# Kernel tuning notes

Hardware: AMD Instinct MI355X
Metric: run time of the kernel (lower is better)

The kernel has to match this reference:

```python
import jax, jax.numpy as jnp
import numpy as np

B, N, FIN = 32, 1024, 6
KCHEB = 3
CLASS_NUM = 40


def _pairwise_adj(x):
    # x: [B, N, D] -> exp(-squared_euclidean_dist) adjacency [B, N, N]
    inner = jnp.einsum('bnd,bmd->bnm', x, x)
    sq = jnp.sum(x * x, axis=-1)
    d2 = sq[:, :, None] - 2.0 * inner + sq[:, None, :]
    return jnp.exp(-d2)


def _get_laplacian(adj):
    # normalized Laplacian: I - D^{-1/2} A D^{-1/2}
    deg = jnp.sum(adj, axis=-1)                       # [B, N]
    d_is = 1.0 / jnp.sqrt(deg)                        # [B, N]
    eye = jnp.eye(adj.shape[-1], dtype=adj.dtype)
    return eye - d_is[:, :, None] * adj * d_is[:, None, :]


def _cheb_conv(x, L, W, b):
    # Chebyshev graph conv: sum_k T_k(L) x W_k + b;  W: [K, Fin, Fout]
    x0 = x
    x1 = jnp.einsum('bnm,bmf->bnf', L, x0)
    out = jnp.einsum('bnf,fg->bng', x0, W[0]) + jnp.einsum('bnf,fg->bng', x1, W[1])
    xk_2, xk_1 = x0, x1
    for k in range(2, W.shape[0]):
        xk = 2.0 * jnp.einsum('bnm,bmf->bnf', L, xk_1) - xk_2
        out = out + jnp.einsum('bnf,fg->bng', xk, W[k])
        xk_2, xk_1 = xk_1, xk
    return out + b


def setup_inputs() -> dict:
    key = jax.random.key(0)
    ks = jax.random.split(key, 16)

    def w(k, shape, fan_in):
        return jax.random.normal(k, shape, dtype=jnp.float32) / np.sqrt(fan_in)

    return {
        'x': jax.random.normal(ks[0], (B, N, FIN), dtype=jnp.float32),
        'W1': w(ks[1], (KCHEB, 6, 128), 6 * KCHEB),
        'b1': jnp.zeros((128,), jnp.float32),
        'W2': w(ks[2], (KCHEB, 128, 512), 128 * KCHEB),
        'b2': jnp.zeros((512,), jnp.float32),
        'W3': w(ks[3], (KCHEB, 512, 1024), 512 * KCHEB),
        'b3': jnp.zeros((1024,), jnp.float32),
        'fc1_w': w(ks[4], (1024, 512), 1024),
        'fc1_b': jnp.zeros((512,), jnp.float32),
        'fc2_w': w(ks[5], (512, 128), 512),
        'fc2_b': jnp.zeros((128,), jnp.float32),
        'fc3_w': w(ks[6], (128, CLASS_NUM), 128),
        'fc3_b': jnp.zeros((CLASS_NUM,), jnp.float32),
    }


def reference(x, W1, b1, W2, b2, W3, b3, fc1_w, fc1_b, fc2_w, fc2_b, fc3_w, fc3_b):
    # Laplacians are computed under torch.no_grad in the original
    L = _get_laplacian(_pairwise_adj(x))
    out = jax.nn.relu(_cheb_conv(x, L, W1, b1))        # [B, N, 128]

    L = _get_laplacian(_pairwise_adj(out))
    out = jax.nn.relu(_cheb_conv(out, L, W2, b2))      # [B, N, 512]

    L = _get_laplacian(_pairwise_adj(out))
    out = jax.nn.relu(_cheb_conv(out, L, W3, b3))      # [B, N, 1024]

    out = jnp.max(out, axis=1)                          # global max pool -> [B, 1024]
    out = jax.nn.relu(out @ fc1_w + fc1_b)              # dropout is identity at eval
    out = jax.nn.relu(out @ fc2_w + fc2_b)
    out = out @ fc3_w + fc3_b                           # [B, CLASS_NUM]
    return out
```

## Files before the change

### kernel.cpp

```cpp
#include <hip/hip_runtime.h>
#include <cstddef>


#define NN 1024

typedef unsigned short ushort_t;
typedef __bf16 bf16x8 __attribute__((ext_vector_type(8)));
typedef float f32x4 __attribute__((ext_vector_type(4)));

__device__ inline ushort_t f2bf(float f) {
    unsigned int u = __float_as_uint(f);
    u = (u + 0x7fffu + ((u >> 16) & 1u)) >> 16;
    return (ushort_t)u;
}
__device__ inline float bf2f(ushort_t s) {
    return __uint_as_float(((unsigned int)s) << 16);
}

__device__ __attribute__((always_inline)) inline void gld16(
    const ushort_t* g, ushort_t* l) {
    __builtin_amdgcn_global_load_lds(
        (__attribute__((address_space(1))) void*)(ushort_t*)g,
        (__attribute__((address_space(3))) void*)l, 16, 0, 0);
}

__global__ void zero_kernel(float* __restrict__ p, int n) {
    int i = blockIdx.x * blockDim.x + threadIdx.x;
    if (i < n) p[i] = 0.f;
}

__global__ __launch_bounds__(256) void wconvT_kernel(
    const float* __restrict__ W, ushort_t* __restrict__ Wt, int Fi, int Fo, int Ks) {
    int p = blockIdx.z;
    int k0 = blockIdx.y * 64, g0 = blockIdx.x * 64;
    __shared__ float T[64][65];
    int t = threadIdx.x;
#pragma unroll
    for (int q = 0; q < 16; ++q) {
        int kr = (t >> 6) + 4 * q, gc = t & 63;
        int k = k0 + kr, g = g0 + gc;
        T[kr][gc] = (k < Fi && g < Fo) ? W[((size_t)p * Fi + k) * Fo + g] : 0.f;
    }
    __syncthreads();
#pragma unroll
    for (int q = 0; q < 16; ++q) {
        int gr = (t >> 6) + 4 * q, kc = t & 63;
        int g = g0 + gr, k = k0 + kc;
        if (g < Fo && k < Ks)
            Wt[((size_t)p * Fo + g) * Ks + k] = f2bf(T[kc][gr]);
    }
}

__global__ __launch_bounds__(256) void prep2_kernel(
    const float* __restrict__ X, ushort_t* __restrict__ hi, ushort_t* __restrict__ lo,
    ushort_t* __restrict__ Xt, float* __restrict__ sq, int F, int Fp, int bsh) {
    int L = blockIdx.x;
    int b = L & ((1 << bsh) - 1), n0 = (L >> bsh) * 64;
    int t = threadIdx.x;
    __shared__ float T[64][65];
    __shared__ float red[4][64];
    const float* Xb = X + ((size_t)b * NN + n0) * F;
    float sacc = 0.f;

    for (int f0 = 0; f0 < Fp; f0 += 64) {
        __syncthreads();
#pragma unroll
        for (int p = 0; p < 16; ++p) {
            int nr = (t >> 6) + 4 * p, fc = t & 63;
            int f = f0 + fc;
            T[nr][fc] = (f < F) ? Xb[(size_t)nr * F + f] : 0.f;
        }
        __syncthreads();
#pragma unroll
        for (int p = 0; p < 16; ++p) {
            int nr = (t >> 6) + 4 * p, fc = t & 63;
            int f = f0 + fc;
            if (f < Fp) {
                float x = T[nr][fc];
                ushort_t h = f2bf(x);
                size_t off = ((size_t)b * NN + n0 + nr) * Fp + f;
                hi[off] = h;
                lo[off] = f2bf(x - bf2f(h));
            }
        }
#pragma unroll
        for (int p = 0; p < 16; ++p) {
            int fr = (t >> 6) + 4 * p;
            int f = f0 + fr;
            if (f < F)
                Xt[((size_t)b * Fp + f) * NN + n0 + (t & 63)] = f2bf(T[t & 63][fr]);
        }
        {
            int nl = t & 63, fq = t >> 6;
#pragma unroll
            for (int fc = 0; fc < 16; ++fc) {
                float v = T[nl][fq * 16 + fc];
                sacc += v * v;
            }
        }
    }
    red[t >> 6][t & 63] = sacc;
    __syncthreads();
    if (t < 64)
        sq[(size_t)b * NN + n0 + t] = red[0][t] + red[1][t] + red[2][t] + red[3][t];
}

__global__ __launch_bounds__(256) void adj_kernel(
    const ushort_t* __restrict__ hi, const ushort_t* __restrict__ lo,
    const float* __restrict__ sq, ushort_t* __restrict__ Abf,
    float* __restrict__ deg_part, int Fp, int bsh, int BCv) {
    int t = threadIdx.x;
    int L = blockIdx.x;
    int b = L & ((1 << bsh) - 1);
    int rest = L >> bsh;
    int ti = 0;
    while (rest >= 8 - ti) { rest -= 8 - ti; ++ti; }
    int tj = ti + rest;
    int n0 = ti * 128, m0 = tj * 128;
    const ushort_t* Hb = hi + (size_t)b * NN * Fp;
    const ushort_t* Lb = lo + (size_t)b * NN * Fp;
    ushort_t* Ab = Abf + (size_t)b * NN * NN;
    const float* sqb = sq + (size_t)b * NN;

    int lane = t & 63, quad = lane >> 4, l16 = lane & 15, wave = t >> 6;
    int rowoff = (wave >> 1) * 64, coloff = (wave & 1) * 64;

    __shared__ __align__(16) ushort_t smem[40960];

    f32x4 acc[4][4];
#pragma unroll
    for (int i = 0; i < 4; ++i)
#pragma unroll
        for (int j = 0; j < 4; ++j) acc[i][j] = (f32x4){0.f, 0.f, 0.f, 0.f};

    int rr0 = t >> 2, kq = (t & 3) * 8;
    int rr1 = rr0 + 64;
    const ushort_t* pAh0 = Hb + (size_t)(n0 + rr0) * Fp + kq;
    const ushort_t* pAh1 = Hb + (size_t)(n0 + rr1) * Fp + kq;
    const ushort_t* pAl0 = Lb + (size_t)(n0 + rr0) * Fp + kq;
    const ushort_t* pAl1 = Lb + (size_t)(n0 + rr1) * Fp + kq;
    const ushort_t* pBh0 = Hb + (size_t)(m0 + rr0) * Fp + kq;
    const ushort_t* pBh1 = Hb + (size_t)(m0 + rr1) * Fp + kq;
    const ushort_t* pBl0 = Lb + (size_t)(m0 + rr0) * Fp + kq;
    const ushort_t* pBl1 = Lb + (size_t)(m0 + rr1) * Fp + kq;
    int o0 = rr0 * 40 + kq, o1 = rr1 * 40 + kq;

    {
        *(uint4*)&smem[o0]         = *(const uint4*)pAh0;
        *(uint4*)&smem[o1]         = *(const uint4*)pAh1;
        *(uint4*)&smem[5120 + o0]  = *(const uint4*)pAl0;
        *(uint4*)&smem[5120 + o1]  = *(const uint4*)pAl1;
        *(uint4*)&smem[10240 + o0] = *(const uint4*)pBh0;
        *(uint4*)&smem[10240 + o1] = *(const uint4*)pBh1;
        *(uint4*)&smem[15360 + o0] = *(const uint4*)pBl0;
        *(uint4*)&smem[15360 + o1] = *(const uint4*)pBl1;
    }
    __syncthreads();

    int NIT = Fp >> 5;
    for (int it = 0; it < NIT; ++it) {
        int cur = (it & 1) * 20480;
        int nxt = 20480 - cur;
        uint4 rh0, rh1, rl0, rl1, sh0, sh1, sl0, sl1;
        if (it + 1 < NIT) {
            int k = (it + 1) * 32;
            rh0 = *(const uint4*)(pAh0 + k); rh1 = *(const uint4*)(pAh1 + k);
            rl0 = *(const uint4*)(pAl0 + k); rl1 = *(const uint4*)(pAl1 + k);
            sh0 = *(const uint4*)(pBh0 + k); sh1 = *(const uint4*)(pBh1 + k);
            sl0 = *(const uint4*)(pBl0 + k); sl1 = *(const uint4*)(pBl1 + k);
        }
        ushort_t* Ah = smem + cur;
        ushort_t* Al = smem + cur + 5120;
        ushort_t* Bh = smem + cur + 10240;
        ushort_t* Bl = smem + cur + 15360;
        bf16x8 ah[4], al[4], bh[4], bl[4];
#pragma unroll
        for (int i = 0; i < 4; ++i) {
            ah[i] = *(const bf16x8*)&Ah[(rowoff + i * 16 + l16) * 40 + quad * 8];
            al[i] = *(const bf16x8*)&Al[(rowoff + i * 16 + l16) * 40 + quad * 8];
        }
#pragma unroll
        for (int j = 0; j < 4; ++j) {
            bh[j] = *(const bf16x8*)&Bh[(coloff + j * 16 + l16) * 40 + quad * 8];
            bl[j] = *(const bf16x8*)&Bl[(coloff + j * 16 + l16) * 40 + quad * 8];
        }
#pragma unroll
        for (int i = 0; i < 4; ++i)
#pragma unroll
            for (int j = 0; j < 4; ++j) {
                acc[i][j] = __builtin_amdgcn_mfma_f32_16x16x32_bf16(al[i], bh[j], acc[i][j], 0, 0, 0);
                acc[i][j] = __builtin_amdgcn_mfma_f32_16x16x32_bf16(ah[i], bl[j], acc[i][j], 0, 0, 0);
                acc[i][j] = __builtin_amdgcn_mfma_f32_16x16x32_bf16(ah[i], bh[j], acc[i][j], 0, 0, 0);
            }
        if (it + 1 < NIT) {
            *(uint4*)&smem[nxt + o0]         = rh0;
            *(uint4*)&smem[nxt + o1]         = rh1;
            *(uint4*)&smem[nxt + 5120 + o0]  = rl0;
            *(uint4*)&smem[nxt + 5120 + o1]  = rl1;
            *(uint4*)&smem[nxt + 10240 + o0] = sh0;
            *(uint4*)&smem[nxt + 10240 + o1] = sh1;
            *(uint4*)&smem[nxt + 15360 + o0] = sl0;
            *(uint4*)&smem[nxt + 15360 + o1] = sl1;
        }
        __syncthreads();
    }

    bool offdiag = (ti != tj);
    float rs[4][4];
    float cs[4] = {0.f, 0.f, 0.f, 0.f};
#pragma unroll
    for (int i = 0; i < 4; ++i)
#pragma unroll
        for (int r = 0; r < 4; ++r) rs[i][r] = 0.f;

#pragma unroll
    for (int j = 0; j < 4; ++j) {
        int ml = coloff + j * 16 + l16;
        int m = m0 + ml;
        float sm = sqb[m];
#pragma unroll
        for (int i = 0; i < 4; ++i) {
#pragma unroll
            for (int r = 0; r < 4; ++r) {
                int nl = rowoff + i * 16 + quad * 4 + r;
                int n = n0 + nl;
                float v = __expf(2.f * acc[i][j][r] - sqb[n] - sm);
                Ab[(size_t)n * NN + m] = f2bf(v);
                rs[i][r] += v;
                if (offdiag) {
                    cs[j] += v;
                    smem[ml * 128 + (((nl >> 3) ^ (ml & 7)) << 3) + (nl & 7)] = f2bf(v);
                }
            }
        }
    }
    int slot = tj * 2 + (wave & 1);
#pragma unroll
    for (int i = 0; i < 4; ++i)
#pragma unroll
        for (int r = 0; r < 4; ++r) {
            float s = rs[i][r];
            s += __shfl_xor(s, 1);
            s += __shfl_xor(s, 2);
            s += __shfl_xor(s, 4);
            s += __shfl_xor(s, 8);
            if (l16 == 0)
                deg_part[((size_t)slot * BCv + b) * NN + n0 + rowoff + i * 16 + quad * 4 + r] = s;
        }

    if (offdiag) {
#pragma unroll
        for (int j = 0; j < 4; ++j) {
            float s = cs[j];
            s += __shfl_xor(s, 16);
            s += __shfl_xor(s, 32);
            cs[j] = s;
        }
        if (quad == 0) {
#pragma unroll
            for (int j = 0; j < 4; ++j)
                deg_part[((size_t)(ti * 2 + (wave >> 1)) * BCv + b) * NN +
                         m0 + coloff + j * 16 + l16] = cs[j];
        }
        __syncthreads();
        for (int s2 = t; s2 < 2048; s2 += 256) {
            int ml = s2 >> 4, oct = s2 & 15;
            uint4 v4 = *(const uint4*)&smem[ml * 128 + ((oct ^ (ml & 7)) << 3)];
            *(uint4*)(Ab + (size_t)(m0 + ml) * NN + n0 + oct * 8) = v4;
        }
    }
}

__global__ __launch_bounds__(256) void disscale_kernel(
    ushort_t* __restrict__ Xt, const float* __restrict__ deg_part,
    float* __restrict__ dis, int Fp, int bsh, int BCv) {
    int L = blockIdx.x;
    int b = L & ((1 << bsh) - 1), n0 = (L >> bsh) * 64;
    int t = threadIdx.x;
    __shared__ float dloc[64];
    if (t < 64) {
        float s = 0.f;
#pragma unroll
        for (int k = 0; k < 16; ++k) s += deg_part[((size_t)k * BCv + b) * NN + n0 + t];
        float d = rsqrtf(s);
        dloc[t] = d;
        dis[(size_t)b * NN + n0 + t] = d;
    }
    __syncthreads();
    int lane = t & 63, fq = t >> 6;
    float d = dloc[lane];
    ushort_t* Xb = Xt + (size_t)b * Fp * NN + n0 + lane;
    for (int f = fq; f < Fp; f += 4) {
        size_t off = (size_t)f * NN;
        Xb[off] = f2bf(bf2f(Xb[off]) * d);
    }
}

__global__ __launch_bounds__(256) void lx_kernel(
    const ushort_t* __restrict__ Abf, const float* __restrict__ dis,
    const ushort_t* __restrict__ in_t, const ushort_t* __restrict__ x0t,
    ushort_t* __restrict__ out_t, ushort_t* __restrict__ out_b,
    int F, int Fp, int mode, int ft, int bsh) {
    int t = threadIdx.x;
    int L = blockIdx.x;
    int b = L & ((1 << bsh) - 1);
    int rest = L >> bsh;
    int m0 = (rest % ft) * 128;
    int n0 = (rest / ft) * 64;
    const ushort_t* Ain = in_t + (size_t)b * Fp * NN;
    const ushort_t* Ab = Abf + (size_t)b * NN * NN;

    int lane = t & 63, quad = lane >> 4, l16 = lane & 15, wave = t >> 6;
    int rowoff = wave * 32;

    __shared__ __align__(16) ushort_t smem[18432];

    f32x4 acc[2][4];
#pragma unroll
    for (int i = 0; i < 2; ++i)
#pragma unroll
        for (int j = 0; j < 4; ++j) acc[i][j] = (f32x4){0.f, 0.f, 0.f, 0.f};

    int lr = lane >> 2, lk = (lane & 3) * 8;
    int rbase = wave * 32;
    const ushort_t* gA = Ain + (size_t)(m0 + rbase + lr) * NN + lk;
    const ushort_t* gB = Ab + (size_t)(n0 + wave * 16 + lr) * NN + lk;

#define LX_STAGE(BOFF, CI)                                            \
    {                                                                 \
        int k_ = (CI) * 32;                                           \
        ushort_t* As_ = smem + (BOFF);                                \
        gld16(gA + k_, As_ + rbase * 32);                             \
        gld16(gA + (size_t)16 * NN + k_, As_ + rbase * 32 + 512);     \
        gld16(gB + k_, As_ + 4096 + wave * 16 * 32);                  \
    }
#define LX_COMP(BOFF)                                                            \
    {                                                                            \
        ushort_t* As_ = smem + (BOFF);                                           \
        ushort_t* Bs_ = As_ + 4096;                                              \
        bf16x8 af[2], bfv[4];                                                    \
        _Pragma("unroll")                                                        \
        for (int i = 0; i < 2; ++i)                                              \
            af[i] = *(const bf16x8*)&As_[(rowoff + i * 16 + l16) * 32 + quad * 8]; \
        _Pragma("unroll")                                                        \
        for (int j = 0; j < 4; ++j)                                              \
            bfv[j] = *(const bf16x8*)&Bs_[(j * 16 + l16) * 32 + quad * 8];       \
        _Pragma("unroll")                                                        \
        for (int i = 0; i < 2; ++i)                                              \
            _Pragma("unroll")                                                    \
            for (int j = 0; j < 4; ++j)                                          \
                acc[i][j] = __builtin_amdgcn_mfma_f32_16x16x32_bf16(af[i], bfv[j], acc[i][j], 0, 0, 0); \
    }

    LX_STAGE(0, 0);
    LX_STAGE(6144, 1);
    int cur = 0;
    for (int ci = 0; ci < 32; ++ci) {
        if (ci < 31) { asm volatile("s_waitcnt vmcnt(3)" ::: "memory"); }
        else         { asm volatile("s_waitcnt vmcnt(0)" ::: "memory"); }
        __builtin_amdgcn_s_barrier();
        asm volatile("" ::: "memory");
        if (ci + 2 < 32) {
            int noff = cur + 12288; if (noff >= 18432) noff -= 18432;
            LX_STAGE(noff, ci + 2);
        }
        LX_COMP(cur);
        cur += 6144; if (cur >= 18432) cur = 0;
    }
#undef LX_STAGE
#undef LX_COMP
    __syncthreads();

#pragma unroll
    for (int j = 0; j < 4; ++j) {
        int nl = j * 16 + l16;
        int n = n0 + nl;
        float dn = dis[(size_t)b * NN + n];
        float inv = 1.f / dn;
        float dn2 = dn * dn;
#pragma unroll
        for (int i = 0; i < 2; ++i) {
#pragma unroll
            for (int r = 0; r < 4; ++r) {
                int fl = rowoff + i * 16 + quad * 4 + r;
                int f = m0 + fl;
                float o = 0.f;
                if (f < F) {
                    float a = acc[i][j][r];
                    size_t off = (size_t)f * NN + n;
                    float xin = bf2f(Ain[off]);
                    if (mode == 0) {
                        out_t[(size_t)b * Fp * NN + off] = f2bf(xin - dn2 * a);
                        o = inv * xin - dn * a;
                    } else {
                        float x0 = bf2f(x0t[(size_t)b * Fp * NN + off]);
                        o = inv * (2.f * xin - x0) - 2.f * dn * a;
                    }
                }
                smem[nl * 128 + (((fl >> 3) ^ (nl & 7)) << 3) + (fl & 7)] = f2bf(o);
            }
        }
    }
    __syncthreads();
    for (int s2 = t; s2 < 1024; s2 += 256) {
        int nl = s2 >> 4, oct = s2 & 15;
        int fg = m0 + oct * 8;
        if (fg < Fp) {
            uint4 v = *(const uint4*)&smem[nl * 128 + ((oct ^ (nl & 7)) << 3)];
            *(uint4*)(out_b + ((size_t)b * NN + n0 + nl) * Fp + fg) = v;
        }
    }
}

__global__ __launch_bounds__(512) void proj_kernel(
    const ushort_t* __restrict__ X0, const ushort_t* __restrict__ X1,
    const ushort_t* __restrict__ X2, const ushort_t* __restrict__ Wt,
    const float* __restrict__ bias, float* __restrict__ O, float* __restrict__ pool,
    int Fp, int Fo, int b0, int n_g, int bsh) {
    int t = threadIdx.x;
    int L = blockIdx.x;
    int c = L & ((1 << bsh) - 1);
    int rest = L >> bsh;
    int g0 = (rest % n_g) * 128;
    int r0 = (c * 4 + rest / n_g) * 256;
    int lane = t & 63, quad = lane >> 4, l16 = lane & 15, wave = t >> 6;
    int rowoff = (wave >> 1) * 64, coloff = (wave & 1) * 64;

    __shared__ __align__(16) ushort_t smem[36864];

    f32x4 acc[4][4];
#pragma unroll
    for (int i = 0; i < 4; ++i)
#pragma unroll
        for (int j = 0; j < 4; ++j) acc[i][j] = (f32x4){0.f, 0.f, 0.f, 0.f};

    int lr = lane >> 2, lk = (lane & 3) * 8;
    int nk = Fp >> 5;
    int NIT = 3 * nk;
    size_t FoFp = (size_t)Fo * Fp;
    size_t r16 = (size_t)16 * Fp;

#define PJ_STAGE(BOFF, CI)                                                    \
    {                                                                         \
        int p_ = (CI) / nk;                                                   \
        int k_ = ((CI) - p_ * nk) * 32 + lk;                                  \
        const ushort_t* Xp_ = (p_ == 0) ? X0 : ((p_ == 1) ? X1 : X2);         \
        const ushort_t* ga_ = Xp_ + (size_t)(r0 + wave * 32 + lr) * Fp + k_;  \
        const ushort_t* gb_ = Wt + (size_t)p_ * FoFp +                        \
                              (size_t)(g0 + wave * 16 + lr) * Fp + k_;        \
        ushort_t* As_ = smem + (BOFF) + wave * 1024;                          \
        ushort_t* Bs_ = smem + (BOFF) + 8192 + wave * 512;                    \
        gld16(ga_, As_);                                                      \
        gld16(ga_ + r16, As_ + 512);                                          \
        gld16(gb_, Bs_);                                                      \
    }
#define PJ_COMP(BOFF)                                                           \
    {                                                                           \
        ushort_t* As_ = smem + (BOFF);                                          \
        ushort_t* Bs_ = As_ + 8192;                                             \
        bf16x8 af[4], bfv[4];                                                   \
        _Pragma("unroll")                                                       \
        for (int i = 0; i < 4; ++i)                                             \
            af[i] = *(const bf16x8*)&As_[(rowoff + i * 16 + l16) * 32 + quad * 8];  \
        _Pragma("unroll")                                                       \
        for (int j = 0; j < 4; ++j)                                             \
            bfv[j] = *(const bf16x8*)&Bs_[(coloff + j * 16 + l16) * 32 + quad * 8]; \
        _Pragma("unroll")                                                       \
        for (int i = 0; i < 4; ++i)                                             \
            _Pragma("unroll")                                                   \
            for (int j = 0; j < 4; ++j)                                         \
                acc[i][j] = __builtin_amdgcn_mfma_f32_16x16x32_bf16(af[i], bfv[j], acc[i][j], 0, 0, 0); \
    }

    PJ_STAGE(0, 0);
    PJ_STAGE(12288, 1);
    int cur = 0;
    for (int ci = 0; ci < NIT; ++ci) {
        if (ci < NIT - 1) { asm volatile("s_waitcnt vmcnt(3)" ::: "memory"); }
        else              { asm volatile("s_waitcnt vmcnt(0)" ::: "memory"); }
        __builtin_amdgcn_s_barrier();
        asm volatile("" ::: "memory");
        if (ci + 2 < NIT) {
            int noff = cur + 24576; if (noff >= 36864) noff -= 36864;
            PJ_STAGE(noff, ci + 2);
        }
        PJ_COMP(cur);
        cur += 12288; if (cur >= 36864) cur = 0;
    }
#undef PJ_STAGE
#undef PJ_COMP

    float bias_l[4];
#pragma unroll
    for (int j = 0; j < 4; ++j) bias_l[j] = bias[g0 + coloff + j * 16 + l16];

    if (O) {
#pragma unroll
        for (int i = 0; i < 4; ++i) {
#pragma unroll
            for (int r = 0; r < 4; ++r) {
                int row = r0 + rowoff + i * 16 + quad * 4 + r;
#pragma unroll
                for (int j = 0; j < 4; ++j) {
                    int g = g0 + coloff + j * 16 + l16;
                    O[(size_t)row * Fo + g] = fmaxf(acc[i][j][r] + bias_l[j], 0.f);
                }
            }
        }
    } else {
        float mj[4];
#pragma unroll
        for (int j = 0; j < 4; ++j) {
            float m = 0.f;
#pragma unroll
            for (int i = 0; i < 4; ++i)
#pragma unroll
                for (int r = 0; r < 4; ++r)
                    m = fmaxf(m, acc[i][j][r] + bias_l[j]);
            m = fmaxf(m, 0.f);
            m = fmaxf(m, __shfl_xor(m, 16));
            m = fmaxf(m, __shfl_xor(m, 32));
            mj[j] = m;
        }
        if (quad == 0) {
            int smp = b0 + (r0 >> 10);
#pragma unroll
            for (int j = 0; j < 4; ++j)
                atomicMax((int*)&pool[(size_t)smp * 1024 + g0 + coloff + j * 16 + l16],
                          __float_as_int(mj[j]));
        }
    }
}

__global__ __launch_bounds__(256) void fc_kernel(
    const float* __restrict__ In, const float* __restrict__ W,
    const float* __restrict__ bias, float* __restrict__ out,
    int K, int Nout, int relu) {
    int r = blockIdx.y;
    int c0 = blockIdx.x * 64;
    int t = threadIdx.x;
    int cl = t & 63, ks = t >> 6;
    int c = c0 + cl;
    int kchunk = K >> 2;
    int k0 = ks * kchunk, k1 = k0 + kchunk;
    float s = 0.f;
    if (c < Nout) {
        const float* ip = In + (size_t)r * K;
        const float* wp = W + c;
#pragma unroll 4
        for (int k = k0; k < k1; ++k) s += ip[k] * wp[(size_t)k * Nout];
    }
    __shared__ float red[4][64];
    red[ks][cl] = s;
    __syncthreads();
    if (t < 64 && c0 + t < Nout) {
        float v = red[0][t] + red[1][t] + red[2][t] + red[3][t] + bias[c0 + t];
        if (relu) v = fmaxf(v, 0.f);
        out[(size_t)r * Nout + c0 + t] = v;
    }
}

extern "C" void kernel_launch(void* const* d_in, const int* in_sizes, int n_in,
                              void* d_out, int out_size, void* d_ws, size_t ws_size,
                              hipStream_t stream) {
    const float* x    = (const float*)d_in[0];
    const float* W1   = (const float*)d_in[1];
    const float* b1   = (const float*)d_in[2];
    const float* W2   = (const float*)d_in[3];
    const float* b2   = (const float*)d_in[4];
    const float* W3   = (const float*)d_in[5];
    const float* b3   = (const float*)d_in[6];
    const float* fc1w = (const float*)d_in[7];
    const float* fc1b = (const float*)d_in[8];
    const float* fc2w = (const float*)d_in[9];
    const float* fc2b = (const float*)d_in[10];
    const float* fc3w = (const float*)d_in[11];
    const float* fc3b = (const float*)d_in[12];
    float* out = (float*)d_out;

    auto need = [](size_t BCv) -> size_t {
        size_t us = (size_t)BCv * 1024;
        return 2 * (us * 1024) + 10 * (us * 512) + 2 * 1781760ull +
               4 * (us * 128) + 4 * (us * 512) + 4 * us + 64 * us + 4 * us +
               4 * (32768ull + 16384 + 4096) + 256;
    };
    int BCv = (ws_size >= need(32)) ? 32 : (ws_size >= need(16)) ? 16 : 8;
    int NCH = 32 / BCv;
    int bsh = (BCv == 32) ? 5 : (BCv == 16) ? 4 : 3;

    size_t usc = (size_t)BCv * 1024;
    size_t Asz = usc * 1024;
    size_t SLv = usc * 512;
    ushort_t* Abf  = (ushort_t*)d_ws;
    ushort_t* X0hi = Abf + Asz;
    ushort_t* X0lo = X0hi + SLv;
    ushort_t* X0t  = X0lo + SLv;
    ushort_t* X1t  = X0t + SLv;
    ushort_t* X1b  = X1t + SLv;
    ushort_t* Wt   = X1b + SLv;
    float* O1   = (float*)(Wt + 1781760);
    float* O2   = O1 + usc * 128;
    float* sq   = O2 + usc * 512;
    float* degp = sq + usc;
    float* dis  = degp + 16 * usc;
    float* pool = dis + usc;
    float* f1   = pool + 32768;
    float* f2   = f1 + 16384;
    ushort_t* X2b = X0lo;

    wconvT_kernel<<<dim3(2, 1, 3), 256, 0, stream>>>(W1, Wt, 6, 128, 32);
    wconvT_kernel<<<dim3(8, 2, 3), 256, 0, stream>>>(W2, Wt + 12288, 128, 512, 128);
    wconvT_kernel<<<dim3(16, 8, 3), 256, 0, stream>>>(W3, Wt + 208896, 512, 1024, 512);
    zero_kernel<<<128, 256, 0, stream>>>(pool, 32768);

    for (int c = 0; c < NCH; ++c) {
        int b0 = c * BCv;
        struct LayerDef {
            const float* X; int F, Fp, Fo;
            const ushort_t* Wtl; const float* bias; float* O;
        };
        LayerDef L[3] = {
            { x + (size_t)b0 * NN * 6, 6,   32,  128,  Wt,          b1, O1 },
            { O1,                      128, 128, 512,  Wt + 12288,  b2, O2 },
            { O2,                      512, 512, 1024, Wt + 208896, b3, nullptr },
        };
        for (int li = 0; li < 3; ++li) {
            LayerDef& Ld = L[li];
            int F = Ld.F, Fp = Ld.Fp;
            int ft = (F + 127) / 128;
            int n_g = Ld.Fo / 128;
            prep2_kernel<<<16 * BCv, 256, 0, stream>>>(Ld.X, X0hi, X0lo, X0t, sq, F, Fp, bsh);
            adj_kernel<<<36 * BCv, 256, 0, stream>>>(X0hi, X0lo, sq, Abf, degp, Fp, bsh, BCv);
            disscale_kernel<<<16 * BCv, 256, 0, stream>>>(X0t, degp, dis, Fp, bsh, BCv);
            lx_kernel<<<ft * 16 * BCv, 256, 0, stream>>>(
                Abf, dis, X0t, nullptr, X1t, X1b, F, Fp, 0, ft, bsh);
            lx_kernel<<<ft * 16 * BCv, 256, 0, stream>>>(
                Abf, dis, X1t, X0t, nullptr, X2b, F, Fp, 1, ft, bsh);
            proj_kernel<<<n_g * 4 * BCv, 512, 0, stream>>>(
                X0hi, X1b, X2b, Ld.Wtl, Ld.bias, Ld.O, pool, Fp, Ld.Fo, b0, n_g, bsh);
        }
    }

    fc_kernel<<<dim3(8, 32), 256, 0, stream>>>(pool, fc1w, fc1b, f1, 1024, 512, 1);
    fc_kernel<<<dim3(2, 32), 256, 0, stream>>>(f1, fc2w, fc2b, f2, 512, 128, 1);
    fc_kernel<<<dim3(1, 32), 256, 0, stream>>>(f2, fc3w, fc3b, out, 128, 40, 0);
}
```

Measured before the change: 959.1 us.

## Emit next-layer bf16 hi/lo split directly from projection epilogue

The projection kernel now writes its ReLU output as bf16 hi/lo pairs instead of fp32, straight into rotating workspace slots. The next layer's prep kernel reads those pairs back and rebuilds the values rather than re-splitting fp32 and rewriting hi/lo. This removes the fp32 intermediate buffers, cuts some memory traffic and shrinks the workspace requirement, which may allow a larger batch chunk. The cost is a buffer permutation across layers with aliasing that must stay correct, and 16-bit scattered stores in the epilogue.

```diff
diff --git a/kernel.cpp b/kernel.cpp
--- a/kernel.cpp
+++ b/kernel.cpp
@@ -59,7 +59,9 @@
     int t = threadIdx.x;
     __shared__ float T[64][65];
     __shared__ float red[4][64];
-    const float* Xb = X + ((size_t)b * NN + n0) * F;
+    const float* Xb = X ? (X + ((size_t)b * NN + n0) * F) : nullptr;
+    const ushort_t* hb = hi + ((size_t)b * NN + n0) * Fp;
+    const ushort_t* lb = lo + ((size_t)b * NN + n0) * Fp;
     float sacc = 0.f;
 
     for (int f0 = 0; f0 < Fp; f0 += 64) {
@@ -68,19 +70,29 @@
         for (int p = 0; p < 16; ++p) {
             int nr = (t >> 6) + 4 * p, fc = t & 63;
             int f = f0 + fc;
-            T[nr][fc] = (f < F) ? Xb[(size_t)nr * F + f] : 0.f;
+            float xv = 0.f;
+            if (f < F) {
+                if (Xb) xv = Xb[(size_t)nr * F + f];
+                else {
+                    size_t off = (size_t)nr * Fp + f;
+                    xv = bf2f(hb[off]) + bf2f(lb[off]);
+                }
+            }
+            T[nr][fc] = xv;
         }
         __syncthreads();
-#pragma unroll
-        for (int p = 0; p < 16; ++p) {
-            int nr = (t >> 6) + 4 * p, fc = t & 63;
-            int f = f0 + fc;
-            if (f < Fp) {
-                float x = T[nr][fc];
-                ushort_t h = f2bf(x);
-                size_t off = ((size_t)b * NN + n0 + nr) * Fp + f;
-                hi[off] = h;
-                lo[off] = f2bf(x - bf2f(h));
+        if (Xb) {
+#pragma unroll
+            for (int p = 0; p < 16; ++p) {
+                int nr = (t >> 6) + 4 * p, fc = t & 63;
+                int f = f0 + fc;
+                if (f < Fp) {
+                    float x = T[nr][fc];
+                    ushort_t h = f2bf(x);
+                    size_t off = ((size_t)b * NN + n0 + nr) * Fp + f;
+                    hi[off] = h;
+                    lo[off] = f2bf(x - bf2f(h));
+                }
             }
         }
 #pragma unroll
@@ -415,7 +427,8 @@
 __global__ __launch_bounds__(512) void proj_kernel(
     const ushort_t* __restrict__ X0, const ushort_t* __restrict__ X1,
     const ushort_t* __restrict__ X2, const ushort_t* __restrict__ Wt,
-    const float* __restrict__ bias, float* __restrict__ O, float* __restrict__ pool,
+    const float* __restrict__ bias, ushort_t* __restrict__ Ohi,
+    ushort_t* __restrict__ Olo, float* __restrict__ pool,
     int Fp, int Fo, int b0, int n_g, int bsh) {
     int t = threadIdx.x;
     int L = blockIdx.x;
@@ -494,7 +507,7 @@
 #pragma unroll
     for (int j = 0; j < 4; ++j) bias_l[j] = bias[g0 + coloff + j * 16 + l16];
 
-    if (O) {
+    if (Ohi) {
 #pragma unroll
         for (int i = 0; i < 4; ++i) {
 #pragma unroll
@@ -503,7 +516,11 @@
 #pragma unroll
                 for (int j = 0; j < 4; ++j) {
                     int g = g0 + coloff + j * 16 + l16;
-                    O[(size_t)row * Fo + g] = fmaxf(acc[i][j][r] + bias_l[j], 0.f);
+                    float o = fmaxf(acc[i][j][r] + bias_l[j], 0.f);
+                    ushort_t h = f2bf(o);
+                    size_t off = (size_t)row * Fo + g;
+                    Ohi[off] = h;
+                    Olo[off] = f2bf(o - bf2f(h));
                 }
             }
         }
@@ -581,7 +598,7 @@
     auto need = [](size_t BCv) -> size_t {
         size_t us = (size_t)BCv * 1024;
         return 2 * (us * 1024) + 10 * (us * 512) + 2 * 1781760ull +
-               4 * (us * 128) + 4 * (us * 512) + 4 * us + 64 * us + 4 * us +
+               4 * us + 64 * us + 4 * us +
                4 * (32768ull + 16384 + 4096) + 256;
     };
     int BCv = (ws_size >= need(32)) ? 32 : (ws_size >= need(16)) ? 16 : 8;
@@ -591,53 +608,59 @@
     size_t usc = (size_t)BCv * 1024;
     size_t Asz = usc * 1024;
     size_t SLv = usc * 512;
-    ushort_t* Abf  = (ushort_t*)d_ws;
-    ushort_t* X0hi = Abf + Asz;
-    ushort_t* X0lo = X0hi + SLv;
-    ushort_t* X0t  = X0lo + SLv;
-    ushort_t* X1t  = X0t + SLv;
-    ushort_t* X1b  = X1t + SLv;
-    ushort_t* Wt   = X1b + SLv;
-    float* O1   = (float*)(Wt + 1781760);
-    float* O2   = O1 + usc * 128;
-    float* sq   = O2 + usc * 512;
+    ushort_t* Abf = (ushort_t*)d_ws;
+    ushort_t* S[5];
+    S[0] = Abf + Asz;
+    for (int i = 1; i < 5; ++i) S[i] = S[i - 1] + SLv;
+    ushort_t* Wt = S[4] + SLv;
+    float* sq   = (float*)(Wt + 1781760);
     float* degp = sq + usc;
     float* dis  = degp + 16 * usc;
     float* pool = dis + usc;
     float* f1   = pool + 32768;
     float* f2   = f1 + 16384;
-    ushort_t* X2b = X0lo;
 
     wconvT_kernel<<<dim3(2, 1, 3), 256, 0, stream>>>(W1, Wt, 6, 128, 32);
     wconvT_kernel<<<dim3(8, 2, 3), 256, 0, stream>>>(W2, Wt + 12288, 128, 512, 128);
     wconvT_kernel<<<dim3(16, 8, 3), 256, 0, stream>>>(W3, Wt + 208896, 512, 1024, 512);
     zero_kernel<<<128, 256, 0, stream>>>(pool, 32768);
 
+    const int MP[3][5] = {{0, 1, 2, 3, 4}, {3, 2, 0, 4, 1}, {4, 0, 3, 1, 2}};
+
     for (int c = 0; c < NCH; ++c) {
         int b0 = c * BCv;
         struct LayerDef {
-            const float* X; int F, Fp, Fo;
-            const ushort_t* Wtl; const float* bias; float* O;
+            int F, Fp, Fo;
+            const ushort_t* Wtl; const float* bias;
         };
         LayerDef L[3] = {
-            { x + (size_t)b0 * NN * 6, 6,   32,  128,  Wt,          b1, O1 },
-            { O1,                      128, 128, 512,  Wt + 12288,  b2, O2 },
-            { O2,                      512, 512, 1024, Wt + 208896, b3, nullptr },
+            { 6,   32,  128,  Wt,          b1 },
+            { 128, 128, 512,  Wt + 12288,  b2 },
+            { 512, 512, 1024, Wt + 208896, b3 },
         };
         for (int li = 0; li < 3; ++li) {
             LayerDef& Ld = L[li];
             int F = Ld.F, Fp = Ld.Fp;
             int ft = (F + 127) / 128;
             int n_g = Ld.Fo / 128;
-            prep2_kernel<<<16 * BCv, 256, 0, stream>>>(Ld.X, X0hi, X0lo, X0t, sq, F, Fp, bsh);
-            adj_kernel<<<36 * BCv, 256, 0, stream>>>(X0hi, X0lo, sq, Abf, degp, Fp, bsh, BCv);
-            disscale_kernel<<<16 * BCv, 256, 0, stream>>>(X0t, degp, dis, Fp, bsh, BCv);
+            ushort_t* xhi = S[MP[li][0]];
+            ushort_t* xlo = S[MP[li][1]];
+            ushort_t* Xt  = S[MP[li][2]];
+            ushort_t* X1t = S[MP[li][3]];
+            ushort_t* X1b = S[MP[li][4]];
+            prep2_kernel<<<16 * BCv, 256, 0, stream>>>(
+                (li == 0) ? (x + (size_t)b0 * NN * 6) : nullptr,
+                xhi, xlo, Xt, sq, F, Fp, bsh);
+            adj_kernel<<<36 * BCv, 256, 0, stream>>>(xhi, xlo, sq, Abf, degp, Fp, bsh, BCv);
+            disscale_kernel<<<16 * BCv, 256, 0, stream>>>(Xt, degp, dis, Fp, bsh, BCv);
             lx_kernel<<<ft * 16 * BCv, 256, 0, stream>>>(
-                Abf, dis, X0t, nullptr, X1t, X1b, F, Fp, 0, ft, bsh);
+                Abf, dis, Xt, nullptr, X1t, X1b, F, Fp, 0, ft, bsh);
             lx_kernel<<<ft * 16 * BCv, 256, 0, stream>>>(
-                Abf, dis, X1t, X0t, nullptr, X2b, F, Fp, 1, ft, bsh);
+                Abf, dis, X1t, Xt, nullptr, xlo, F, Fp, 1, ft, bsh);
             proj_kernel<<<n_g * 4 * BCv, 512, 0, stream>>>(
-                X0hi, X1b, X2b, Ld.Wtl, Ld.bias, Ld.O, pool, Fp, Ld.Fo, b0, n_g, bsh);
+                xhi, X1b, xlo, Ld.Wtl, Ld.bias,
+                (li < 2) ? X1t : nullptr, (li < 2) ? Xt : nullptr,
+                pool, Fp, Ld.Fo, b0, n_g, bsh);
         }
     }
 
```

Result: faster. 812.4 us (-15.3%).
